# Kernel optimization log

Measured on AMD Instinct MI355X. Metric: run time of the kernel, lower is better.

The kernel has to match this reference:

```python
import jax, jax.numpy as jnp
import numpy as np

B, LQ, LK = 4, 1024, 1024
D, H, FF = 1024, 16, 4096
DH = D // H
NREL = 32
NEG = jnp.float32(-1e9)


def _layer_norm(x, g, b, eps=1e-5):
    m = x.mean(-1, keepdims=True)
    v = x.var(-1, keepdims=True)
    return (x - m) * jax.lax.rsqrt(v + eps) * g + b


def _mha_rel_eb(xq, xkv, rel_ids, mask, wq, bq, wk, bk, wv, bv, wo, bo, rel_k, rel_b):
    # Shaw-style relative attention with relative key embeddings (rel-e)
    # and relative position biases (rel-b): the 'rel-eb' variant.
    Bb, Lq, _ = xq.shape
    Lk = xkv.shape[1]
    q = (xq @ wq.T + bq).reshape(Bb, Lq, H, DH).transpose(0, 2, 1, 3)   # bhqd
    k = (xkv @ wk.T + bk).reshape(Bb, Lk, H, DH).transpose(0, 2, 1, 3)  # bhkd
    v = (xkv @ wv.T + bv).reshape(Bb, Lk, H, DH).transpose(0, 2, 1, 3)  # bhkd
    scores = jnp.einsum('bhqd,bhkd->bhqk', q, k)
    ek = rel_k[rel_ids]                                  # [Lq,Lk,DH] gather
    scores = scores + jnp.einsum('bhqd,qkd->bhqk', q, ek)
    scores = scores + rel_b[rel_ids].transpose(2, 0, 1)[None]  # [1,H,Lq,Lk]
    scores = scores / jnp.sqrt(jnp.float32(DH))
    scores = jnp.where(mask, scores, NEG)
    attn = jax.nn.softmax(scores, axis=-1)
    out = jnp.einsum('bhqk,bhkd->bqhd', attn, v).reshape(Bb, Lq, D)
    return out @ wo.T + bo


def setup_inputs() -> dict:
    key = jax.random.key(0)
    ks = jax.random.split(key, 40)
    i = iter(range(40))
    nrm = lambda shape, s=0.02: jax.random.normal(ks[next(i)], shape, jnp.float32) * s
    inp = {}
    inp['x'] = jax.random.normal(ks[next(i)], (B, LQ, D), jnp.float32)
    inp['enc_output'] = jax.random.normal(ks[next(i)], (B, LK, D), jnp.float32)
    inp['dec_relative_ids1'] = jax.random.randint(ks[next(i)], (LQ, LQ), 0, NREL)
    inp['dec2enc_relative_ids'] = jax.random.randint(ks[next(i)], (LQ, LK), 0, NREL)
    inp['trg_mask'] = jnp.tril(jnp.ones((LQ, LQ), bool))[None, None]  # causal decoder mask
    inp['src_mask'] = jnp.ones((1, 1, LQ, LK), bool)
    for s in ('1', '2'):  # self (1) and cross (2) attention params
        for nm in ('wq', 'wk', 'wv', 'wo'):
            inp[nm + s] = nrm((D, D))
        for nm in ('bq', 'bk', 'bv', 'bo'):
            inp[nm + s] = jnp.zeros((D,), jnp.float32)
        inp['rel_k' + s] = nrm((NREL, DH))
        inp['rel_b' + s] = nrm((NREL, H))
    inp['w1'] = nrm((FF, D))
    inp['b1'] = jnp.zeros((FF,), jnp.float32)
    inp['w2'] = nrm((D, FF))
    inp['b2'] = jnp.zeros((D,), jnp.float32)
    for s in ('1', '2', '3'):
        inp['g' + s] = jnp.ones((D,), jnp.float32)
        inp['be' + s] = jnp.zeros((D,), jnp.float32)
    return inp


def reference(x, enc_output, dec_relative_ids1, dec2enc_relative_ids, trg_mask, src_mask,
              wq1, wk1, wv1, wo1, bq1, bk1, bv1, bo1, rel_k1, rel_b1,
              wq2, wk2, wv2, wo2, bq2, bk2, bv2, bo2, rel_k2, rel_b2,
              w1, b1, w2, b2, g1, be1, g2, be2, g3, be3):
    a = _mha_rel_eb(x, x, dec_relative_ids1, trg_mask,
                    wq1, bq1, wk1, bk1, wv1, bv1, wo1, bo1, rel_k1, rel_b1)
    x = _layer_norm(x + a, g1, be1)
    a = _mha_rel_eb(x, enc_output, dec2enc_relative_ids, src_mask,
                    wq2, bq2, wk2, bk2, wv2, bv2, wo2, bo2, rel_k2, rel_b2)
    x = _layer_norm(x + a, g2, be2)
    ff = jax.nn.relu(x @ w1.T + b1) @ w2.T + b2
    return _layer_norm(x + ff, g3, be3)
```

## Files before the change

### kernel.cpp

```cpp
#include <hip/hip_runtime.h>
#include <cstdint>
#include <cstddef>

#define DEV static __device__ __forceinline__

constexpr int Bn = 4, LQ = 1024, Dm = 1024, Hh = 16, FFd = 4096, DHd = 64, NR = 32;
constexpr int ROWS = Bn * LQ;

typedef __attribute__((ext_vector_type(8))) short v8s;
typedef __attribute__((ext_vector_type(4))) float v4f;

DEV float bf2f(ushort u) { union { uint32_t i; float f; } w; w.i = ((uint32_t)u) << 16; return w.f; }
DEV ushort f2bf(float f) {
  union { float f; uint32_t i; } w; w.f = f;
  uint32_t r = w.i + 0x7fffu + ((w.i >> 16) & 1u);
  return (ushort)(r >> 16);
}
DEV uint32_t asu(float f) { union { float f; uint32_t i; } w; w.f = f; return w.i; }

struct CvtArgs {
  const float* src[14];
  ushort* dst[14];
  int cum[15];
};
__global__ __launch_bounds__(256)
void k_cvt_all(CvtArgs a) {
  int t = blockIdx.x * 256 + threadIdx.x;
  if (t >= a.cum[14]) return;
  int seg = 0;
#pragma unroll
  for (int s = 1; s < 14; s++) if (t >= a.cum[s]) seg = s;
  int u = t - a.cum[seg];
  float4 v = *(const float4*)(a.src[seg] + (size_t)u * 4);
  ushort4 w; w.x = f2bf(v.x); w.y = f2bf(v.y); w.z = f2bf(v.z); w.w = f2bf(v.w);
  *(ushort4*)(a.dst[seg] + (size_t)u * 4) = w;
}

__global__ __launch_bounds__(256)
void k_bias(const float* __restrict__ bq1, const float* __restrict__ bk1, const float* __restrict__ bv1,
            const float* __restrict__ bk2, const float* __restrict__ bv2,
            float* __restrict__ o1, float* __restrict__ o2) {
  int t = blockIdx.x * 256 + threadIdx.x;
  if (t < 3072) o1[t] = t < 1024 ? bq1[t] : (t < 2048 ? bk1[t - 1024] : bv1[t - 2048]);
  else if (t < 5120) { int u = t - 3072; o2[u] = u < 1024 ? bk2[u] : bv2[u - 1024]; }
}

__global__ __launch_bounds__(256)
void k_ids8(const int* __restrict__ i1, const int* __restrict__ i2,
            unsigned char* __restrict__ o1, unsigned char* __restrict__ o2) {
  int t = blockIdx.x * 256 + threadIdx.x;
  const int n = LQ * LQ / 4;
  if (t >= 2 * n) return;
  const int* ip = t < n ? i1 : i2;
  unsigned char* op = t < n ? o1 : o2;
  int u = t < n ? t : t - n;
  int q = u >> 8;
  int k4 = (u & 255) * 4;
  int4 v = *(const int4*)(ip + (size_t)q * LQ + k4);
  uchar4 pk; pk.x = (unsigned char)v.x; pk.y = (unsigned char)v.y;
  pk.z = (unsigned char)v.z; pk.w = (unsigned char)v.w;
  *(uchar4*)(op + (size_t)q * LQ + k4) = pk;
}

template<int OUT>
__global__ __launch_bounds__(256)
void k_gemm(const ushort* __restrict__ A, const ushort* __restrict__ Bw,
            const float* __restrict__ bias, void* __restrict__ Cp,
            int M, int N, int K) {
  constexpr int BM = 128, BN = 128, BK = 32;
  __shared__ __align__(16) ushort As[BM * BK];
  __shared__ __align__(16) ushort Bs[BN * BK];
  const int tm = blockIdx.y * BM, tn = blockIdx.x * BN;
  const int tid = threadIdx.x;
  const int wave = tid >> 6, lane = tid & 63;
  const int wm = (wave & 1) * 64, wn = (wave >> 1) * 64;
  const int lr = lane & 15, lqd = lane >> 4;
  v4f acc[4][4];
#pragma unroll
  for (int i = 0; i < 4; i++)
#pragma unroll
    for (int j = 0; j < 4; j++) acc[i][j] = (v4f){0.f, 0.f, 0.f, 0.f};

  for (int k0 = 0; k0 < K; k0 += BK) {
#pragma unroll
    for (int s = 0; s < 2; s++) {
      int c = s * 256 + tid;
      int row = c >> 2, kc = c & 3;
      const ushort* ga = A + (size_t)(tm + row) * K + k0 + kc * 8;
      const ushort* gb = Bw + (size_t)(tn + row) * K + k0 + kc * 8;
      int ldsoff = (s * 256 + wave * 64) * 8;
      __builtin_amdgcn_global_load_lds((const __attribute__((address_space(1))) void*)ga,
                                       (__attribute__((address_space(3))) void*)(As + ldsoff), 16, 0, 0);
      __builtin_amdgcn_global_load_lds((const __attribute__((address_space(1))) void*)gb,
                                       (__attribute__((address_space(3))) void*)(Bs + ldsoff), 16, 0, 0);
    }
    __syncthreads();
    v8s af[4], bfr[4];
#pragma unroll
    for (int i = 0; i < 4; i++)
      af[i] = *(const v8s*)(As + (wm + i * 16 + lr) * BK + lqd * 8);
#pragma unroll
    for (int i = 0; i < 4; i++)
      bfr[i] = *(const v8s*)(Bs + (wn + i * 16 + lr) * BK + lqd * 8);
#pragma unroll
    for (int i = 0; i < 4; i++)
#pragma unroll
      for (int j = 0; j < 4; j++)
        acc[i][j] = __builtin_amdgcn_mfma_f32_16x16x32_bf16(af[i], bfr[j], acc[i][j], 0, 0, 0);
    __syncthreads();
  }
#pragma unroll
  for (int i = 0; i < 4; i++) {
#pragma unroll
    for (int j = 0; j < 4; j++) {
      int col = tn + wn + j * 16 + lr;
      float bv = bias[col];
#pragma unroll
      for (int r = 0; r < 4; r++) {
        int row = tm + wm + i * 16 + lqd * 4 + r;
        float v = acc[i][j][r] + bv;
        if (OUT == 2) v = fmaxf(v, 0.f);
        if (OUT == 0) ((float*)Cp)[(size_t)row * N + col] = v;
        else          ((ushort*)Cp)[(size_t)row * N + col] = f2bf(v);
      }
    }
  }
}

template<bool CAUSAL>
__global__ __launch_bounds__(256)
void k_flash(const ushort* __restrict__ Q, const ushort* __restrict__ Kv,
             const ushort* __restrict__ Vv, const ushort* __restrict__ relkb,
             const float* __restrict__ relb, const unsigned char* __restrict__ ids8,
             ushort* __restrict__ Out, int Lk, int ldq, int ldkv) {
  constexpr int ST = 72;
  __shared__ __align__(16) ushort Ks[2][64 * 64];
  __shared__ __align__(16) ushort Vt[DHd * ST];
  __shared__ __align__(16) ushort Ps[64 * ST];
  __shared__ __align__(16) unsigned char ids_s[2][64 * 64];
  __shared__ float qb_s[64 * 33];
  const int bh = blockIdx.y, b = bh >> 4, h = bh & 15;
  const int q0 = blockIdx.x * 64;
  const int tid = threadIdx.x, wave = tid >> 6, lane = tid & 63;
  const int lr = lane & 15, quad = lane >> 4;
  const int phi = lr >> 1;
  const int rq = tid >> 4, cc = tid & 15;
  const ushort* Qb = Q + (size_t)b * LQ * ldq + h * DHd;
  const ushort* Kb = Kv + (size_t)b * Lk * ldkv + h * DHd;
  const ushort* Vb = Vv + (size_t)b * Lk * ldkv + h * DHd;

  v8s qf0 = *(const v8s*)(Qb + (size_t)(q0 + wave * 16 + lr) * ldq + quad * 8);
  v8s qf1 = *(const v8s*)(Qb + (size_t)(q0 + wave * 16 + lr) * ldq + 32 + quad * 8);

  auto dmaK = [&](int k0v, int bufi) {
#pragma unroll
    for (int s = 0; s < 2; s++) {
      int c = s * 256 + wave * 64 + lane;
      int row = c >> 3;
      int kc = (c & 7) ^ ((c >> 6) & 7);
      const ushort* g0 = Kb + (size_t)(k0v + row) * ldkv + kc * 8;
      __builtin_amdgcn_global_load_lds((const __attribute__((address_space(1))) void*)g0,
          (__attribute__((address_space(3))) void*)(&Ks[bufi][0] + (s * 256 + wave * 64) * 8), 16, 0, 0);
    }
  };
  auto dmaI = [&](int k0v, int bufi) {
    int c = wave * 64 + lane;
    int row = c >> 2, seg = c & 3;
    const unsigned char* g = ids8 + (size_t)(q0 + row) * Lk + k0v + seg * 16;
    __builtin_amdgcn_global_load_lds((const __attribute__((address_space(1))) void*)g,
        (__attribute__((address_space(3))) void*)(ids_s[bufi] + wave * 1024), 16, 0, 0);
  };
  ushort4 vr[4];
  auto loadV = [&](int k0v) {
    const ushort* vp = Vb + (size_t)(k0v + rq * 4) * ldkv + cc * 4;
#pragma unroll
    for (int i = 0; i < 4; i++) vr[i] = *(const ushort4*)(vp + (size_t)i * ldkv);
  };
  auto writeVt = [&]() {
    ushort4 w0 = {vr[0].x, vr[1].x, vr[2].x, vr[3].x};
    ushort4 w1 = {vr[0].y, vr[1].y, vr[2].y, vr[3].y};
    ushort4 w2 = {vr[0].z, vr[1].z, vr[2].z, vr[3].z};
    ushort4 w3 = {vr[0].w, vr[1].w, vr[2].w, vr[3].w};
    *(ushort4*)(Vt + (cc * 4 + 0) * ST + rq * 4) = w0;
    *(ushort4*)(Vt + (cc * 4 + 1) * ST + rq * 4) = w1;
    *(ushort4*)(Vt + (cc * 4 + 2) * ST + rq * 4) = w2;
    *(ushort4*)(Vt + (cc * 4 + 3) * ST + rq * 4) = w3;
  };

  dmaK(0, 0); dmaI(0, 0);
  loadV(0);

  {
    v4f z = (v4f){0.f, 0.f, 0.f, 0.f};
    v8s rk0a = *(const v8s*)(relkb + lr * 64 + quad * 8);
    v8s rk0b = *(const v8s*)(relkb + lr * 64 + 32 + quad * 8);
    v8s rk1a = *(const v8s*)(relkb + (lr + 16) * 64 + quad * 8);
    v8s rk1b = *(const v8s*)(relkb + (lr + 16) * 64 + 32 + quad * 8);
    v4f q0r = __builtin_amdgcn_mfma_f32_16x16x32_bf16(qf0, rk0a, z, 0, 0, 0);
    q0r = __builtin_amdgcn_mfma_f32_16x16x32_bf16(qf1, rk0b, q0r, 0, 0, 0);
    v4f q1r = __builtin_amdgcn_mfma_f32_16x16x32_bf16(qf0, rk1a, z, 0, 0, 0);
    q1r = __builtin_amdgcn_mfma_f32_16x16x32_bf16(qf1, rk1b, q1r, 0, 0, 0);
    float rb0 = relb[lr * Hh + h], rb1 = relb[(lr + 16) * Hh + h];
#pragma unroll
    for (int r = 0; r < 4; r++) {
      int q = wave * 16 + quad * 4 + r;
      qb_s[q * 33 + lr] = q0r[r] + rb0;
      qb_s[q * 33 + 16 + lr] = q1r[r] + rb1;
    }
  }

  v4f o[4];
#pragma unroll
  for (int f = 0; f < 4; f++) o[f] = (v4f){0.f, 0.f, 0.f, 0.f};
  float l_[4] = {0.f, 0.f, 0.f, 0.f};

  const int kend = CAUSAL ? (q0 + 64) : Lk;
  const int nit = kend >> 6;
  __syncthreads();

  for (int it = 0; it < nit; it++) {
    const int k0v = it << 6, buf = it & 1;
    const bool more = (it + 1 < nit);
    if (more) { dmaK(k0v + 64, buf ^ 1); dmaI(k0v + 64, buf ^ 1); }
    v4f sa[4];
#pragma unroll
    for (int j = 0; j < 4; j++) {
      const int r = 4 * lr + j;
      const ushort* base = &Ks[buf][0];
      v8s kf0 = *(const v8s*)(base + (r * 8 + (quad ^ phi)) * 8);
      v8s kf1 = *(const v8s*)(base + (r * 8 + ((quad + 4) ^ phi)) * 8);
      v4f z = (v4f){0.f, 0.f, 0.f, 0.f};
      z = __builtin_amdgcn_mfma_f32_16x16x32_bf16(qf0, kf0, z, 0, 0, 0);
      z = __builtin_amdgcn_mfma_f32_16x16x32_bf16(qf1, kf1, z, 0, 0, 0);
      sa[j] = z;
    }
    writeVt();
    if (more) loadV(k0v + 64);
    const bool diag = CAUSAL && (k0v == q0);
    float p[4][4];
#pragma unroll
    for (int r = 0; r < 4; r++) {
      int q = wave * 16 + quad * 4 + r;
      uchar4 idv = *(const uchar4*)(ids_s[buf] + q * 64 + 4 * lr);
      float d0 = (sa[0][r] + qb_s[q * 33 + idv.x]) * 0.125f;
      float d1 = (sa[1][r] + qb_s[q * 33 + idv.y]) * 0.125f;
      float d2 = (sa[2][r] + qb_s[q * 33 + idv.z]) * 0.125f;
      float d3 = (sa[3][r] + qb_s[q * 33 + idv.w]) * 0.125f;
      if (diag) {
        int kb = 4 * lr;
        if (kb + 0 > q) d0 = -1e9f;
        if (kb + 1 > q) d1 = -1e9f;
        if (kb + 2 > q) d2 = -1e9f;
        if (kb + 3 > q) d3 = -1e9f;
      }
      p[r][0] = __expf(fminf(d0, 60.f));
      p[r][1] = __expf(fminf(d1, 60.f));
      p[r][2] = __expf(fminf(d2, 60.f));
      p[r][3] = __expf(fminf(d3, 60.f));
      float ts = (p[r][0] + p[r][1]) + (p[r][2] + p[r][3]);
      ts += __shfl_xor(ts, 1, 64);
      ts += __shfl_xor(ts, 2, 64);
      ts += __shfl_xor(ts, 4, 64);
      ts += __shfl_xor(ts, 8, 64);
      l_[r] += ts;
    }
#pragma unroll
    for (int r = 0; r < 4; r++) {
      int q = wave * 16 + quad * 4 + r;
      uint32_t b0 = asu(p[r][0]) + 0x8000u, b1 = asu(p[r][1]) + 0x8000u;
      uint32_t b2 = asu(p[r][2]) + 0x8000u, b3 = asu(p[r][3]) + 0x8000u;
      uint2 pk;
      pk.x = __builtin_amdgcn_perm(b1, b0, 0x07060302u);
      pk.y = __builtin_amdgcn_perm(b3, b2, 0x07060302u);
      *(uint2*)(Ps + q * ST + 4 * lr) = pk;
    }
    __syncthreads();
    v8s pf0 = *(const v8s*)(Ps + (wave * 16 + lr) * ST + quad * 8);
    v8s pf1 = *(const v8s*)(Ps + (wave * 16 + lr) * ST + 32 + quad * 8);
#pragma unroll
    for (int f = 0; f < 4; f++) {
      v8s vf0 = *(const v8s*)(Vt + (f * 16 + lr) * ST + quad * 8);
      v8s vf1 = *(const v8s*)(Vt + (f * 16 + lr) * ST + 32 + quad * 8);
      o[f] = __builtin_amdgcn_mfma_f32_16x16x32_bf16(pf0, vf0, o[f], 0, 0, 0);
      o[f] = __builtin_amdgcn_mfma_f32_16x16x32_bf16(pf1, vf1, o[f], 0, 0, 0);
    }
    __syncthreads();
  }
#pragma unroll
  for (int r = 0; r < 4; r++) {
    float inv = 1.f / l_[r];
    int qabs = q0 + wave * 16 + quad * 4 + r;
    ushort* op = Out + ((size_t)b * LQ + qabs) * Dm + h * DHd + lr;
#pragma unroll
    for (int f = 0; f < 4; f++)
      op[f * 16] = f2bf(o[f][r] * inv);
  }
}

__global__ __launch_bounds__(256)
void k_addln(const float* __restrict__ res, const ushort* __restrict__ xin,
             const float* __restrict__ gw, const float* __restrict__ bw,
             float* __restrict__ yout, ushort* __restrict__ ybf) {
  const int row = blockIdx.x, t = threadIdx.x;
  float4 a = *(const float4*)(res + (size_t)row * Dm + t * 4);
  ushort4 cu = *(const ushort4*)(xin + (size_t)row * Dm + t * 4);
  float v0 = a.x + bf2f(cu.x), v1 = a.y + bf2f(cu.y), v2 = a.z + bf2f(cu.z), v3 = a.w + bf2f(cu.w);
  float s = v0 + v1 + v2 + v3;
  float q = v0 * v0 + v1 * v1 + v2 * v2 + v3 * v3;
#pragma unroll
  for (int o = 32; o > 0; o >>= 1) { s += __shfl_xor(s, o, 64); q += __shfl_xor(q, o, 64); }
  __shared__ float sb[4], qb[4];
  if ((t & 63) == 0) { sb[t >> 6] = s; qb[t >> 6] = q; }
  __syncthreads();
  s = sb[0] + sb[1] + sb[2] + sb[3];
  q = qb[0] + qb[1] + qb[2] + qb[3];
  const float mean = s * (1.f / Dm);
  const float var = q * (1.f / Dm) - mean * mean;
  const float inv = rsqrtf(var + 1e-5f);
  float4 g4 = *(const float4*)(gw + t * 4);
  float4 b4 = *(const float4*)(bw + t * 4);
  float o0 = (v0 - mean) * inv * g4.x + b4.x;
  float o1 = (v1 - mean) * inv * g4.y + b4.y;
  float o2 = (v2 - mean) * inv * g4.z + b4.z;
  float o3 = (v3 - mean) * inv * g4.w + b4.w;
  float4 o = {o0, o1, o2, o3};
  *(float4*)(yout + (size_t)row * Dm + t * 4) = o;
  if (ybf) {
    ushort4 u; u.x = f2bf(o0); u.y = f2bf(o1); u.z = f2bf(o2); u.w = f2bf(o3);
    *(ushort4*)(ybf + (size_t)row * Dm + t * 4) = u;
  }
}

extern "C" void kernel_launch(void* const* d_in, const int* in_sizes, int n_in,
                              void* d_out, int out_size, void* d_ws, size_t ws_size,
                              hipStream_t stream) {
  (void)in_sizes; (void)n_in; (void)out_size; (void)ws_size;
  const float* x     = (const float*)d_in[0];
  const float* enc   = (const float*)d_in[1];
  const int*   ids1  = (const int*)d_in[2];
  const int*   ids2  = (const int*)d_in[3];
  const float* wq1 = (const float*)d_in[6],  *wk1 = (const float*)d_in[7];
  const float* wv1 = (const float*)d_in[8],  *wo1 = (const float*)d_in[9];
  const float* bq1 = (const float*)d_in[10], *bk1 = (const float*)d_in[11];
  const float* bv1 = (const float*)d_in[12], *bo1 = (const float*)d_in[13];
  const float* relk1 = (const float*)d_in[14], *relb1 = (const float*)d_in[15];
  const float* wq2 = (const float*)d_in[16], *wk2 = (const float*)d_in[17];
  const float* wv2 = (const float*)d_in[18], *wo2 = (const float*)d_in[19];
  const float* bq2 = (const float*)d_in[20], *bk2 = (const float*)d_in[21];
  const float* bv2 = (const float*)d_in[22], *bo2 = (const float*)d_in[23];
  const float* relk2 = (const float*)d_in[24], *relb2 = (const float*)d_in[25];
  const float* w1 = (const float*)d_in[26], *b1 = (const float*)d_in[27];
  const float* w2 = (const float*)d_in[28], *b2 = (const float*)d_in[29];
  const float* g1 = (const float*)d_in[30], *be1 = (const float*)d_in[31];
  const float* g2 = (const float*)d_in[32], *be2 = (const float*)d_in[33];
  const float* g3 = (const float*)d_in[34], *be3 = (const float*)d_in[35];

  char* W = (char*)d_ws;
  const size_t MB = 1u << 20;
  ushort* wqkv1b = (ushort*)(W + 0 * MB);
  ushort* wo1b   = (ushort*)(W + 6 * MB);
  ushort* wq2b   = (ushort*)(W + 8 * MB);
  ushort* wkv2b  = (ushort*)(W + 10 * MB);
  ushort* wo2b   = (ushort*)(W + 14 * MB);
  ushort* w1b    = (ushort*)(W + 16 * MB);
  ushort* w2b    = (ushort*)(W + 24 * MB);
  ushort* xb     = (ushort*)(W + 32 * MB);
  ushort* yb     = (ushort*)(W + 32 * MB);
  ushort* encb   = (ushort*)(W + 40 * MB);
  ushort* qkv    = (ushort*)(W + 48 * MB);
  ushort* q8c    = (ushort*)(W + 48 * MB);
  ushort* ffh    = (ushort*)(W + 48 * MB);
  ushort* kv2    = (ushort*)(W + 80 * MB);
  ushort* t8     = (ushort*)(W + 80 * MB);
  ushort* attb   = (ushort*)(W + 96 * MB);
  ushort* relkb1 = (ushort*)(W + 104 * MB);
  ushort* relkb2 = (ushort*)(W + 104 * MB + 8192);
  unsigned char* ids8a = (unsigned char*)(W + 108 * MB);
  unsigned char* ids8b = (unsigned char*)(W + 109 * MB);
  float* bqkv1   = (float*)(W + 110 * MB);
  float* bkv2    = (float*)(W + 110 * MB + 65536);
  float* y       = (float*)(W + 111 * MB);

  CvtArgs ca;
  const float* srcs[14] = {x, enc, wq1, wk1, wv1, wo1, wq2, wk2, wv2, wo2, w1, w2, relk1, relk2};
  ushort* dsts[14] = {xb, encb, wqkv1b, wqkv1b + 1024 * 1024, wqkv1b + 2 * 1024 * 1024,
                      wo1b, wq2b, wkv2b, wkv2b + 1024 * 1024, wo2b, w1b, w2b, relkb1, relkb2};
  int lens[14] = {ROWS * Dm, ROWS * Dm, Dm * Dm, Dm * Dm, Dm * Dm, Dm * Dm,
                  Dm * Dm, Dm * Dm, Dm * Dm, Dm * Dm, FFd * Dm, Dm * FFd, NR * DHd, NR * DHd};
  int cum = 0;
  for (int i = 0; i < 14; i++) { ca.src[i] = srcs[i]; ca.dst[i] = dsts[i]; ca.cum[i] = cum; cum += lens[i] >> 2; }
  ca.cum[14] = cum;
  k_cvt_all<<<dim3((cum + 255) / 256), 256, 0, stream>>>(ca);
  k_bias<<<dim3(20), 256, 0, stream>>>(bq1, bk1, bv1, bk2, bv2, bqkv1, bkv2);
  k_ids8<<<dim3(2048), 256, 0, stream>>>(ids1, ids2, ids8a, ids8b);

  auto gemm = [&](int mode, const ushort* A, const ushort* Bw, const float* bias,
                  void* C, int M, int N, int K) {
    dim3 g(N / 128, M / 128);
    if (mode == 0)      k_gemm<0><<<g, 256, 0, stream>>>(A, Bw, bias, C, M, N, K);
    else if (mode == 1) k_gemm<1><<<g, 256, 0, stream>>>(A, Bw, bias, C, M, N, K);
    else                k_gemm<2><<<g, 256, 0, stream>>>(A, Bw, bias, C, M, N, K);
  };

  gemm(1, xb, wqkv1b, bqkv1, qkv, ROWS, 3072, Dm);
  k_flash<true><<<dim3(LQ / 64, Bn * Hh), 256, 0, stream>>>(
      qkv, qkv + 1024, qkv + 2048, relkb1, relb1, ids8a, attb, LQ, 3072, 3072);
  gemm(1, attb, wo1b, bo1, t8, ROWS, Dm, Dm);
  k_addln<<<dim3(ROWS), 256, 0, stream>>>(x, t8, g1, be1, y, yb);

  gemm(1, yb, wq2b, bq2, q8c, ROWS, Dm, Dm);
  gemm(1, encb, wkv2b, bkv2, kv2, ROWS, 2048, Dm);
  k_flash<false><<<dim3(LQ / 64, Bn * Hh), 256, 0, stream>>>(
      q8c, kv2, kv2 + 1024, relkb2, relb2, ids8b, attb, LQ, 1024, 2048);
  gemm(1, attb, wo2b, bo2, t8, ROWS, Dm, Dm);
  k_addln<<<dim3(ROWS), 256, 0, stream>>>(y, t8, g2, be2, y, yb);

  gemm(2, yb, w1b, b1, ffh, ROWS, FFd, Dm);
  gemm(1, ffh, w2b, b2, t8, ROWS, Dm, FFd);
  k_addln<<<dim3(ROWS), 256, 0, stream>>>(y, t8, g3, be3, (float*)d_out, nullptr);
}
```

Before: 657.5 us.

## Add 64-row GEMM tiles, XCD-aware block mapping, and packed bf16 stores

Templates the GEMM on tile height, using 64x128 tiles for the N=1024 projections so more blocks fill the CUs. Blocks are remapped from a 1D grid so consecutive column tiles land on the same XCD, aiming for better L2 reuse of weights. Epilogue stores pack two bf16 values per 32-bit write using a lane shuffle. Smaller tiles lower arithmetic intensity per block and add shuffle overhead, and the fp32 output mode is dropped.

```diff
diff --git a/kernel.cpp b/kernel.cpp
--- a/kernel.cpp
+++ b/kernel.cpp
@@ -62,66 +62,80 @@
   *(uchar4*)(op + (size_t)q * LQ + k4) = pk;
 }
 
-template<int OUT>
+template<int OUT, int BM>
 __global__ __launch_bounds__(256)
 void k_gemm(const ushort* __restrict__ A, const ushort* __restrict__ Bw,
             const float* __restrict__ bias, void* __restrict__ Cp,
             int M, int N, int K) {
-  constexpr int BM = 128, BN = 128, BK = 32;
+  constexpr int BN = 128, BK = 32;
+  constexpr int NI = 4, NJ = (BM == 128) ? 4 : 2;
   __shared__ __align__(16) ushort As[BM * BK];
   __shared__ __align__(16) ushort Bs[BN * BK];
-  const int tm = blockIdx.y * BM, tn = blockIdx.x * BN;
+  const int nN = N >> 7, k8 = nN >> 3;
+  const int bid = blockIdx.x;
+  const int xcd = bid & 7, sb = bid >> 3;
+  const int tn = (xcd + ((sb % k8) << 3)) << 7;
+  const int tm = (sb / k8) * BM;
   const int tid = threadIdx.x;
   const int wave = tid >> 6, lane = tid & 63;
-  const int wm = (wave & 1) * 64, wn = (wave >> 1) * 64;
+  const int wm = (BM == 128) ? (wave & 1) * 64 : 0;
+  const int wn = (BM == 128) ? (wave >> 1) * 64 : wave * 32;
   const int lr = lane & 15, lqd = lane >> 4;
-  v4f acc[4][4];
-#pragma unroll
-  for (int i = 0; i < 4; i++)
-#pragma unroll
-    for (int j = 0; j < 4; j++) acc[i][j] = (v4f){0.f, 0.f, 0.f, 0.f};
+  v4f acc[NI][NJ];
+#pragma unroll
+  for (int i = 0; i < NI; i++)
+#pragma unroll
+    for (int j = 0; j < NJ; j++) acc[i][j] = (v4f){0.f, 0.f, 0.f, 0.f};
 
   for (int k0 = 0; k0 < K; k0 += BK) {
+#pragma unroll
+    for (int s = 0; s < BM / 64; s++) {
+      int c = s * 256 + tid;
+      int row = c >> 2, kc = c & 3;
+      const ushort* ga = A + (size_t)(tm + row) * K + k0 + kc * 8;
+      __builtin_amdgcn_global_load_lds((const __attribute__((address_space(1))) void*)ga,
+          (__attribute__((address_space(3))) void*)(As + (s * 256 + wave * 64) * 8), 16, 0, 0);
+    }
 #pragma unroll
     for (int s = 0; s < 2; s++) {
       int c = s * 256 + tid;
       int row = c >> 2, kc = c & 3;
-      const ushort* ga = A + (size_t)(tm + row) * K + k0 + kc * 8;
       const ushort* gb = Bw + (size_t)(tn + row) * K + k0 + kc * 8;
-      int ldsoff = (s * 256 + wave * 64) * 8;
-      __builtin_amdgcn_global_load_lds((const __attribute__((address_space(1))) void*)ga,
-                                       (__attribute__((address_space(3))) void*)(As + ldsoff), 16, 0, 0);
       __builtin_amdgcn_global_load_lds((const __attribute__((address_space(1))) void*)gb,
-                                       (__attribute__((address_space(3))) void*)(Bs + ldsoff), 16, 0, 0);
+          (__attribute__((address_space(3))) void*)(Bs + (s * 256 + wave * 64) * 8), 16, 0, 0);
     }
     __syncthreads();
-    v8s af[4], bfr[4];
-#pragma unroll
-    for (int i = 0; i < 4; i++)
+    v8s af[NI], bfr[NJ];
+#pragma unroll
+    for (int i = 0; i < NI; i++)
       af[i] = *(const v8s*)(As + (wm + i * 16 + lr) * BK + lqd * 8);
 #pragma unroll
-    for (int i = 0; i < 4; i++)
-      bfr[i] = *(const v8s*)(Bs + (wn + i * 16 + lr) * BK + lqd * 8);
-#pragma unroll
-    for (int i = 0; i < 4; i++)
-#pragma unroll
-      for (int j = 0; j < 4; j++)
+    for (int j = 0; j < NJ; j++)
+      bfr[j] = *(const v8s*)(Bs + (wn + j * 16 + lr) * BK + lqd * 8);
+#pragma unroll
+    for (int i = 0; i < NI; i++)
+#pragma unroll
+      for (int j = 0; j < NJ; j++)
         acc[i][j] = __builtin_amdgcn_mfma_f32_16x16x32_bf16(af[i], bfr[j], acc[i][j], 0, 0, 0);
     __syncthreads();
   }
-#pragma unroll
-  for (int i = 0; i < 4; i++) {
-#pragma unroll
-    for (int j = 0; j < 4; j++) {
+  const bool evenl = (lane & 1) == 0;
+#pragma unroll
+  for (int i = 0; i < NI; i++) {
+#pragma unroll
+    for (int j = 0; j < NJ; j++) {
       int col = tn + wn + j * 16 + lr;
       float bv = bias[col];
 #pragma unroll
       for (int r = 0; r < 4; r++) {
-        int row = tm + wm + i * 16 + lqd * 4 + r;
         float v = acc[i][j][r] + bv;
         if (OUT == 2) v = fmaxf(v, 0.f);
-        if (OUT == 0) ((float*)Cp)[(size_t)row * N + col] = v;
-        else          ((ushort*)Cp)[(size_t)row * N + col] = f2bf(v);
+        float vn = __shfl_xor(v, 1, 64);
+        if (evenl) {
+          uint32_t pk = (uint32_t)f2bf(v) | ((uint32_t)f2bf(vn) << 16);
+          int row = tm + wm + i * 16 + lqd * 4 + r;
+          *(uint32_t*)((ushort*)Cp + (size_t)row * N + col) = pk;
+        }
       }
     }
   }
@@ -394,28 +408,31 @@
   k_bias<<<dim3(20), 256, 0, stream>>>(bq1, bk1, bv1, bk2, bv2, bqkv1, bkv2);
   k_ids8<<<dim3(2048), 256, 0, stream>>>(ids1, ids2, ids8a, ids8b);
 
-  auto gemm = [&](int mode, const ushort* A, const ushort* Bw, const float* bias,
+  auto gemm = [&](int mode, int bm, const ushort* A, const ushort* Bw, const float* bias,
                   void* C, int M, int N, int K) {
-    dim3 g(N / 128, M / 128);
-    if (mode == 0)      k_gemm<0><<<g, 256, 0, stream>>>(A, Bw, bias, C, M, N, K);
-    else if (mode == 1) k_gemm<1><<<g, 256, 0, stream>>>(A, Bw, bias, C, M, N, K);
-    else                k_gemm<2><<<g, 256, 0, stream>>>(A, Bw, bias, C, M, N, K);
+    dim3 g((M / bm) * (N / 128));
+    if (bm == 128) {
+      if (mode == 1) k_gemm<1, 128><<<g, 256, 0, stream>>>(A, Bw, bias, C, M, N, K);
+      else           k_gemm<2, 128><<<g, 256, 0, stream>>>(A, Bw, bias, C, M, N, K);
+    } else {
+      k_gemm<1, 64><<<g, 256, 0, stream>>>(A, Bw, bias, C, M, N, K);
+    }
   };
 
-  gemm(1, xb, wqkv1b, bqkv1, qkv, ROWS, 3072, Dm);
+  gemm(1, 128, xb, wqkv1b, bqkv1, qkv, ROWS, 3072, Dm);
   k_flash<true><<<dim3(LQ / 64, Bn * Hh), 256, 0, stream>>>(
       qkv, qkv + 1024, qkv + 2048, relkb1, relb1, ids8a, attb, LQ, 3072, 3072);
-  gemm(1, attb, wo1b, bo1, t8, ROWS, Dm, Dm);
+  gemm(1, 64, attb, wo1b, bo1, t8, ROWS, 1024, Dm);
   k_addln<<<dim3(ROWS), 256, 0, stream>>>(x, t8, g1, be1, y, yb);
 
-  gemm(1, yb, wq2b, bq2, q8c, ROWS, Dm, Dm);
-  gemm(1, encb, wkv2b, bkv2, kv2, ROWS, 2048, Dm);
+  gemm(1, 64, yb, wq2b, bq2, q8c, ROWS, 1024, Dm);
+  gemm(1, 128, encb, wkv2b, bkv2, kv2, ROWS, 2048, Dm);
   k_flash<false><<<dim3(LQ / 64, Bn * Hh), 256, 0, stream>>>(
       q8c, kv2, kv2 + 1024, relkb2, relb2, ids8b, attb, LQ, 1024, 2048);
-  gemm(1, attb, wo2b, bo2, t8, ROWS, Dm, Dm);
+  gemm(1, 64, attb, wo2b, bo2, t8, ROWS, 1024, Dm);
   k_addln<<<dim3(ROWS), 256, 0, stream>>>(y, t8, g2, be2, y, yb);
 
-  gemm(2, yb, w1b, b1, ffh, ROWS, FFd, Dm);
-  gemm(1, ffh, w2b, b2, t8, ROWS, Dm, FFd);
+  gemm(2, 128, yb, w1b, b1, ffh, ROWS, FFd, Dm);
+  gemm(1, 64, ffh, w2b, b2, t8, ROWS, 1024, FFd);
   k_addln<<<dim3(ROWS), 256, 0, stream>>>(y, t8, g3, be3, (float*)d_out, nullptr);
 }
```

Result: no change. 666.2 us (+1.3%).
